# Optimization experiments

Hardware: AMD Instinct MI355X
Metric: run time of the kernel (lower is better)

Reference implementation:

```python
import jax, jax.numpy as jnp
import numpy as np

# ---- static dims (from init_kwargs / Hydra defaults) ----
B_, N_MESH, G, HEADS, DH = 2, 100000, 64, 8, 64
DIM = 256
D_MODEL = HEADS * DH              # 512
EXPAND, D_STATE, D_CONV = 2, 64, 3
D_INNER = EXPAND * D_MODEL        # 1024
HEADDIM = 64
NHEADS = D_INNER // HEADDIM       # 16
CONV_DIM = D_INNER + 2 * D_STATE  # 1152
D_IN_PROJ = 2 * D_INNER + 2 * D_STATE + 2 * NHEADS  # 2208


def _ssd_scan(x, dt, A, B, C):
    """Selective state-space scan (SSD / Mamba2 recurrence).
    x:(bb,L,H,P) dt:(bb,L,H) A:(H,) B,C:(bb,L,N). Returns y:(bb,L,H,P)."""
    bb, L, H, P = x.shape
    N = B.shape[-1]
    xs = jnp.moveaxis(x, 1, 0)   # (L,bb,H,P)
    dts = jnp.moveaxis(dt, 1, 0)  # (L,bb,H)
    Bs = jnp.moveaxis(B, 1, 0)   # (L,bb,N)
    Cs = jnp.moveaxis(C, 1, 0)
    h0 = jnp.zeros((bb, H, P, N), x.dtype)

    def step(h, inp):
        x_t, dt_t, B_t, C_t = inp
        dA = jnp.exp(dt_t * A)                                   # (bb,H)
        h = dA[..., None, None] * h + (dt_t[..., None] * x_t)[..., None] * B_t[:, None, None, :]
        y_t = jnp.einsum('bhpn,bn->bhp', h, C_t)
        return h, y_t

    _, ys = jax.lax.scan(step, h0, (xs, dts, Bs, Cs))
    return jnp.moveaxis(ys, 0, 1)


def _hydra(u, in_proj_w, conv_w, conv_b, dt_bias, A_log, fc_D_w, D, norm_w, out_proj_w):
    """Hydra (bidirectional Mamba2) forward, slow (non mem-eff) path."""
    b, L, _ = u.shape
    zxbcdt = u @ in_proj_w.T                                     # (b,L,2208)
    z = zxbcdt[..., :D_INNER]
    xBC = zxbcdt[..., D_INNER:D_INNER + CONV_DIM]
    dt_raw = zxbcdt[..., D_INNER + CONV_DIM:]                    # (b,L,2*NHEADS)
    # forward heads + time-flipped backward heads stacked along batch
    dt = jnp.concatenate([dt_raw[..., :NHEADS], jnp.flip(dt_raw[..., NHEADS:], axis=1)], axis=0)
    dt = jax.nn.softplus(dt + dt_bias)                           # (2b,L,NHEADS)
    # depthwise non-causal 'same' conv1d + SiLU
    xBC = jax.lax.conv_general_dilated(
        xBC.transpose(0, 2, 1), conv_w, (1,), [(1, 1)],
        dimension_numbers=('NCH', 'OIH', 'NCH'), feature_group_count=CONV_DIM)
    xBC = jax.nn.silu(xBC + conv_b[None, :, None]).transpose(0, 2, 1)
    x = xBC[..., :D_INNER]
    Bc = xBC[..., D_INNER:D_INNER + D_STATE]
    Cc = xBC[..., D_INNER + D_STATE:]
    x_og = x
    x2 = jnp.concatenate([x, jnp.flip(x, 1)], 0).reshape(2 * b, L, NHEADS, HEADDIM)
    B2 = jnp.concatenate([Bc, jnp.flip(Bc, 1)], 0)
    C2 = jnp.concatenate([Cc, jnp.flip(Cc, 1)], 0)
    A = -jnp.exp(A_log)                                          # (NHEADS,)
    y = _ssd_scan(x2, dt, A, B2, C2).reshape(2 * b, L, D_INNER)
    # shift by one (strictly off-diagonal parts), zero first position
    y = jnp.pad(y[:, :-1], ((0, 0), (1, 0), (0, 0)))
    diag = x_og @ fc_D_w.T + D                                   # (b,L,NHEADS)
    y = y[:b] + jnp.flip(y[b:], 1) + x_og * jnp.repeat(diag, HEADDIM, axis=-1)
    # gated RMSNorm
    y = y * jax.nn.silu(z)
    y = y * jax.lax.rsqrt(jnp.mean(y * y, axis=-1, keepdims=True) + 1e-5) * norm_w
    return y @ out_proj_w.T                                      # (b,L,D_MODEL)


def _forward(slice_token, slice_weights, in_proj_w, conv_w, conv_b, dt_bias, A_log,
             fc_D_w, D, norm_w, out_proj_w, to_out_w, to_out_b):
    b, h, g, c = slice_token.shape
    u = slice_token.transpose(0, 2, 1, 3).reshape(b, g, h * c)   # b g (h c)
    out = _hydra(u, in_proj_w, conv_w, conv_b, dt_bias, A_log, fc_D_w, D, norm_w, out_proj_w)
    ost = out.reshape(b, g, h, c).transpose(0, 2, 1, 3)          # b h g c
    out_x = jnp.einsum('bhgc,bhng->bhnc', ost, slice_weights)    # gather back to mesh points
    out_x = out_x.transpose(0, 2, 1, 3).reshape(b, out_x.shape[2], h * c)  # b n (h c)
    return out_x @ to_out_w.T + to_out_b


def setup_inputs() -> dict:
    key = jax.random.key(0)
    ks = jax.random.split(key, 14)
    f32 = jnp.float32
    inp = {}
    inp['slice_token'] = jax.random.normal(ks[0], (B_, HEADS, G, DH), f32)
    inp['slice_weights'] = jax.random.uniform(ks[1], (B_, HEADS, N_MESH, G), f32)
    inp['in_proj_w'] = jax.random.normal(ks[2], (D_IN_PROJ, D_MODEL), f32) * (D_MODEL ** -0.5)
    inp['conv_w'] = jax.random.normal(ks[3], (CONV_DIM, 1, D_CONV), f32) * 0.3
    inp['conv_b'] = jax.random.normal(ks[4], (CONV_DIM,), f32) * 0.02
    inp['dt_bias'] = jnp.log(jnp.expm1(jax.random.uniform(ks[5], (NHEADS,), f32, 0.001, 0.1)))
    inp['A_log'] = jnp.log(jax.random.uniform(ks[6], (NHEADS,), f32, 1.0, 8.0))
    inp['fc_D_w'] = jax.random.normal(ks[7], (NHEADS, D_INNER), f32) * (D_INNER ** -0.5)
    inp['D'] = jax.random.normal(ks[8], (NHEADS,), f32) * 0.1 + 1.0
    inp['norm_w'] = jnp.ones((D_INNER,), f32)
    inp['out_proj_w'] = jax.random.normal(ks[9], (D_MODEL, D_INNER), f32) * (D_INNER ** -0.5)
    inp['to_out_w'] = jax.random.normal(ks[10], (DIM, D_MODEL), f32) * (D_MODEL ** -0.5)
    inp['to_out_b'] = jnp.zeros((DIM,), f32)
    return inp


def reference(slice_token, slice_weights, in_proj_w, conv_w, conv_b, dt_bias, A_log,
              fc_D_w, D, norm_w, out_proj_w, to_out_w, to_out_b):
    return _forward(slice_token, slice_weights, in_proj_w, conv_w, conv_b, dt_bias,
                    A_log, fc_D_w, D, norm_w, out_proj_w, to_out_w, to_out_b)
```

## Files before the change

kernel.cpp:

```cpp
#include <hip/hip_runtime.h>
#include <hip/hip_bf16.h>
#include <math.h>

#define NB 2
#define LL 64
#define NMESH 100000
#define HEADS_O 8
#define DHC 64
#define DMODEL 512
#define DINNER 1024
#define DSTATE 64
#define NH 16
#define CONVDIM 1152
#define DINPROJ 2208
#define DOUT 256
#define NCHUNK 6250

typedef __attribute__((ext_vector_type(8))) short short8v;
typedef __attribute__((ext_vector_type(4))) float f32x4;

__device__ __forceinline__ unsigned short f2bf(float f) {
  union { float f; unsigned u; } v; v.f = f;
  unsigned u = v.u;
  u += 0x7FFFu + ((u >> 16) & 1u);
  return (unsigned short)(u >> 16);
}

__device__ __forceinline__ short8v pack_bf16(float4 lo, float4 hi) {
  short8v r;
  r[0] = (short)f2bf(lo.x); r[1] = (short)f2bf(lo.y);
  r[2] = (short)f2bf(lo.z); r[3] = (short)f2bf(lo.w);
  r[4] = (short)f2bf(hi.x); r[5] = (short)f2bf(hi.y);
  r[6] = (short)f2bf(hi.z); r[7] = (short)f2bf(hi.w);
  return r;
}

__device__ __forceinline__ float dot4(float4 a, const float* b) {
  return a.x*b[0] + a.y*b[1] + a.z*b[2] + a.w*b[3];
}

__device__ __forceinline__ float silu(float s) { return s / (1.f + expf(-s)); }

__global__ void k_inproj(const float* __restrict__ st, const float* __restrict__ w,
                         float* __restrict__ zx) {
  int oc = blockIdx.x;
  int blc = blockIdx.y;
  int t = threadIdx.x;
  __shared__ float u[8][DMODEL];
  for (int idx = t; idx < 8*DMODEL; idx += 256) {
    int r = idx >> 9, m = idx & 511;
    int bl = blc*8 + r; int b = bl >> 6, l = bl & 63;
    u[r][m] = st[((size_t)(b*HEADS_O + (m >> 6))*LL + l)*DHC + (m & 63)];
  }
  __syncthreads();
  int o = oc*256 + t;
  if (o < DINPROJ) {
    const float4* wr = (const float4*)(w + (size_t)o*DMODEL);
    float acc[8] = {0,0,0,0,0,0,0,0};
    for (int m4 = 0; m4 < DMODEL/4; ++m4) {
      float4 wv = wr[m4];
      #pragma unroll
      for (int r = 0; r < 8; ++r) acc[r] += dot4(wv, &u[r][m4*4]);
    }
    #pragma unroll
    for (int r = 0; r < 8; ++r)
      zx[(size_t)(blc*8 + r)*DINPROJ + o] = acc[r];
  }
}

__global__ void k_convdt(const float* __restrict__ zx, const float* __restrict__ cw,
                         const float* __restrict__ cb, const float* __restrict__ dtb,
                         float* __restrict__ conv_out, float* __restrict__ dtbuf) {
  if (blockIdx.x < 576) {
    int i = blockIdx.x*256 + threadIdx.x;
    int c = i % CONVDIM; int l = (i / CONVDIM) % LL; int b = i / (CONVDIM*LL);
    float s = cb[c];
    #pragma unroll
    for (int k = 0; k < 3; ++k) {
      int tt = l - 1 + k;
      if (tt >= 0 && tt < LL)
        s += cw[c*3 + k] * zx[(size_t)(b*LL + tt)*DINPROJ + DINNER + c];
    }
    conv_out[i] = silu(s);
  } else {
    int i = (blockIdx.x - 576)*256 + threadIdx.x;
    if (i < 4*LL*NH) {
      int h = i & 15, l = (i >> 4) & 63, s = i >> 10;
      float v;
      if (s < 2)
        v = zx[(size_t)(s*LL + l)*DINPROJ + (DINNER + CONVDIM) + h];
      else
        v = zx[(size_t)((s-2)*LL + (63-l))*DINPROJ + (DINNER + CONVDIM) + 16 + h];
      v += dtb[h];
      dtbuf[i] = (v > 20.f) ? v : log1pf(expf(v));
    }
  }
}

__global__ void k_scan(const float* __restrict__ conv_out, const float* __restrict__ dtbuf,
                       const float* __restrict__ A_log, float* __restrict__ ybuf) {
  int blk = blockIdx.x;
  int s = blk >> 4, hh = blk & 15;
  int b = s & 1;
  bool rev = (s >= 2);
  int t = threadIdx.x;
  int wv = t >> 6, lane = t & 63;
  __shared__ float Bs[64*68];
  __shared__ float Cs[64*68];
  __shared__ float Xs[64*64];
  __shared__ float dts[64];
  __shared__ float Dc[64];

  for (int id = t; id < 4096; id += 256) {
    int tt0 = id >> 6, n = id & 63;
    int tt = rev ? (63 - tt0) : tt0;
    size_t base = (size_t)(b*LL + tt) * CONVDIM;
    Xs[tt0*64 + n] = conv_out[base + hh*64 + n];
    Bs[tt0*68 + n] = conv_out[base + DINNER + n];
    Cs[tt0*68 + n] = conv_out[base + DINNER + DSTATE + n];
  }
  if (t < 64) dts[t] = dtbuf[(size_t)(s*LL + t)*NH + hh];
  __syncthreads();
  if (t < 64) {
    float v = dts[t];
    #pragma unroll
    for (int m = 1; m < 64; m <<= 1) {
      float o = __shfl_up(v, m, 64);
      if (lane >= m) v += o;
    }
    Dc[t] = v;
  }
  __syncthreads();
  float A = -expf(A_log[hh]);
  float g[16];
  #pragma unroll
  for (int i = 0; i < 16; ++i) {
    int tt = wv + 4*i;
    int ta = lane;
    float gv = 0.f;
    if (ta <= tt) {
      const float* Br = &Bs[ta*68];
      const float* Cr = &Cs[tt*68];
      float dot = 0.f;
      #pragma unroll
      for (int n4 = 0; n4 < 16; ++n4) {
        float4 bv = *(const float4*)&Br[n4*4];
        float4 cv = *(const float4*)&Cr[n4*4];
        dot += bv.x*cv.x + bv.y*cv.y + bv.z*cv.z + bv.w*cv.w;
      }
      gv = dot * expf(A * (Dc[tt] - Dc[ta])) * dts[ta];
    }
    g[i] = gv;
  }
  __syncthreads();
  #pragma unroll
  for (int i = 0; i < 16; ++i) Bs[(wv + 4*i)*64 + lane] = g[i];
  __syncthreads();
  for (int id = t; id < 4096; id += 256) {
    int tt = id >> 6, p = id & 63;
    float y = 0.f;
    for (int ta = 0; ta <= tt; ++ta) y += Bs[tt*64 + ta] * Xs[ta*64 + p];
    ybuf[(size_t)(s*LL + tt)*DINNER + hh*64 + p] = y;
  }
}

__global__ void k_norm(const float* __restrict__ conv_out, const float* __restrict__ zx,
                       const float* __restrict__ yb, const float* __restrict__ fcD,
                       const float* __restrict__ Dd, const float* __restrict__ nw,
                       float* __restrict__ ynorm) {
  int bl = blockIdx.x; int b = bl >> 6, l = bl & 63;
  int t = threadIdx.x;
  __shared__ float xog[DINNER];
  __shared__ float diag[NH];
  __shared__ float wsum[4];
  size_t base = (size_t)bl * CONVDIM;
  for (int c = t; c < DINNER; c += 256) xog[c] = conv_out[base + c];
  __syncthreads();
  {
    int hh = t >> 4, j = t & 15;
    const float* fr = fcD + (size_t)hh*DINNER;
    float acc = 0.f;
    for (int k = 0; k < 64; ++k) acc += xog[j + 16*k] * fr[j + 16*k];
    #pragma unroll
    for (int m = 8; m >= 1; m >>= 1) acc += __shfl_xor(acc, m, 64);
    if (j == 0) diag[hh] = acc + Dd[hh];
  }
  __syncthreads();
  float ss = 0.f;
  float y2v[4];
  #pragma unroll
  for (int i = 0; i < 4; ++i) {
    int c = t + 256*i;
    float yf = (l == 0)  ? 0.f : yb[(size_t)(b*LL + l - 1)*DINNER + c];
    float yw = (l == 63) ? 0.f : yb[(size_t)((2+b)*LL + 62 - l)*DINNER + c];
    float y1 = yf + yw + xog[c]*diag[c >> 6];
    float z = zx[(size_t)bl*DINPROJ + c];
    float y2 = y1 * silu(z);
    y2v[i] = y2;
    ss += y2*y2;
  }
  #pragma unroll
  for (int m = 32; m >= 1; m >>= 1) ss += __shfl_xor(ss, m, 64);
  if ((t & 63) == 0) wsum[t >> 6] = ss;
  __syncthreads();
  float tot = wsum[0] + wsum[1] + wsum[2] + wsum[3];
  float scale = rsqrtf(tot * (1.f/1024.f) + 1e-5f);
  #pragma unroll
  for (int i = 0; i < 4; ++i) {
    int c = t + 256*i;
    ynorm[(size_t)bl*DINNER + c] = y2v[i] * scale * nw[c];
  }
}

__global__ void k_oproj(const float* __restrict__ ynorm, const float* __restrict__ opw,
                        float* __restrict__ oh) {
  int oc = blockIdx.x;
  int blc = blockIdx.y;
  int t = threadIdx.x;
  __shared__ float yr[4][DINNER];
  for (int idx = t; idx < 4*DINNER; idx += 256) {
    int r = idx >> 10, k = idx & 1023;
    yr[r][k] = ynorm[(size_t)(blc*4 + r)*DINNER + k];
  }
  __syncthreads();
  int o = oc*256 + t;
  const float4* wr = (const float4*)(opw + (size_t)o*DINNER);
  float acc[4] = {0,0,0,0};
  for (int k4 = 0; k4 < DINNER/4; ++k4) {
    float4 wv = wr[k4];
    #pragma unroll
    for (int r = 0; r < 4; ++r) acc[r] += dot4(wv, &yr[r][k4*4]);
  }
  #pragma unroll
  for (int r = 0; r < 4; ++r)
    oh[(size_t)(blc*4 + r)*DMODEL + o] = acc[r];
}

__global__ void k_mfrag(const float* __restrict__ oh, const float* __restrict__ tow,
                        unsigned short* __restrict__ mfp) {
  int bgc = blockIdx.x;
  int dc  = blockIdx.y;
  int t = threadIdx.x;
  __shared__ float orow[8][DMODEL];
  for (int idx = t; idx < 8*DMODEL; idx += 256) {
    int r = idx >> 9, m = idx & 511;
    orow[r][m] = oh[(size_t)(bgc*8 + r)*DMODEL + m];
  }
  __syncthreads();
  #pragma unroll
  for (int ii = 0; ii < 2; ++ii) {
    int idx = t + 256*ii;
    int h = idx >> 6, dl = idx & 63;
    int d = dc*64 + dl;
    const float4* wr = (const float4*)(tow + (size_t)d*DMODEL + h*64);
    float acc[8] = {0,0,0,0,0,0,0,0};
    #pragma unroll
    for (int c4 = 0; c4 < 16; ++c4) {
      float4 wv = wr[c4];
      #pragma unroll
      for (int r = 0; r < 8; ++r) acc[r] += dot4(wv, &orow[r][h*64 + c4*4]);
    }
    #pragma unroll
    for (int r = 0; r < 8; ++r) {
      int bg = bgc*8 + r; int b = bg >> 6, g = bg & 63;
      int kk = g >> 5;
      int ln = (d & 15) | (((g & 31) >> 3) << 4);
      int j = g & 7;
      mfp[((((size_t)(b*HEADS_O + h)*2 + kk)*16 + (d >> 4))*64 + ln)*8 + j] = f2bf(acc[r]);
    }
  }
}

__global__ __launch_bounds__(512, 1) void k_out_gemm(const float* __restrict__ W,
                                                     const unsigned short* __restrict__ mf,
                                                     const float* __restrict__ tob,
                                                     float* __restrict__ out) {
  int bx = blockIdx.x;
  int b    = bx >> 7;
  int base = bx & 127;
  int tid = threadIdx.x;
  int wv = tid >> 6, lane = tid & 63;
  int r16 = lane & 15, kg = lane >> 4;

  __shared__ __align__(16) unsigned short lsA[2][16][512];

  short8v B0[16], B1[16];
  {
    const unsigned short* mfb = mf + (size_t)b*(16*16*512) + lane*8;
    #pragma unroll
    for (int ks = 0; ks < 16; ++ks) {
      B0[ks] = *(const short8v*)(mfb + ((size_t)ks*16 + 2*wv    )*512);
      B1[ks] = *(const short8v*)(mfb + ((size_t)ks*16 + 2*wv + 1)*512);
    }
  }
  float bias0 = tob[wv*32 + r16];
  float bias1 = tob[wv*32 + 16 + r16];

  const float* wbase = W + ((size_t)(b*HEADS_O + wv)*NMESH + r16)*64 + kg*8;

  float4 s00, s01, s10, s11;
  #define ALOAD(cc) do { \
    const float* p0 = wbase + (size_t)(cc)*1024; \
    s00 = *(const float4*)p0;        s01 = *(const float4*)(p0 + 4); \
    s10 = *(const float4*)(p0 + 32); s11 = *(const float4*)(p0 + 36); \
  } while (0)
  #define AWRITE(pp) do { \
    *(short8v*)&lsA[pp][2*wv    ][lane*8] = pack_bf16(s00, s01); \
    *(short8v*)&lsA[pp][2*wv + 1][lane*8] = pack_bf16(s10, s11); \
  } while (0)

  ALOAD(base);
  AWRITE(0);
  asm volatile("s_waitcnt lgkmcnt(0)" ::: "memory");
  __builtin_amdgcn_sched_barrier(0);
  __builtin_amdgcn_s_barrier();
  __builtin_amdgcn_sched_barrier(0);

  int c = base;
  int p = 0;
  for (;;) {
    int cn = c + 128;
    bool more = (cn < NCHUNK);
    if (more) ALOAD(cn);
    __builtin_amdgcn_sched_barrier(0);

    f32x4 acc0 = (f32x4){0.f,0.f,0.f,0.f};
    f32x4 acc1 = (f32x4){0.f,0.f,0.f,0.f};
    #pragma unroll
    for (int ks = 0; ks < 16; ++ks) {
      short8v af = *(const short8v*)&lsA[p][ks][lane*8];
      acc0 = __builtin_amdgcn_mfma_f32_16x16x32_bf16(af, B0[ks], acc0, 0, 0, 0);
      acc1 = __builtin_amdgcn_mfma_f32_16x16x32_bf16(af, B1[ks], acc1, 0, 0, 0);
    }

    int rb = c*16 + kg*4;
    int cg = wv*32 + r16;
    #pragma unroll
    for (int r = 0; r < 4; ++r) {
      out[((size_t)b*NMESH + rb + r)*DOUT + cg]      = acc0[r] + bias0;
      out[((size_t)b*NMESH + rb + r)*DOUT + cg + 16] = acc1[r] + bias1;
    }

    if (!more) break;
    __builtin_amdgcn_sched_barrier(0);
    AWRITE(p ^ 1);
    asm volatile("s_waitcnt lgkmcnt(0)" ::: "memory");
    __builtin_amdgcn_sched_barrier(0);
    __builtin_amdgcn_s_barrier();
    __builtin_amdgcn_sched_barrier(0);
    p ^= 1;
    c = cn;
  }
  #undef ALOAD
  #undef AWRITE
}

extern "C" void kernel_launch(void* const* d_in, const int* in_sizes, int n_in,
                              void* d_out, int out_size, void* d_ws, size_t ws_size,
                              hipStream_t stream) {
  (void)in_sizes; (void)n_in; (void)out_size; (void)ws_size;
  const float* st   = (const float*)d_in[0];
  const float* sw   = (const float*)d_in[1];
  const float* ipw  = (const float*)d_in[2];
  const float* cw   = (const float*)d_in[3];
  const float* cb   = (const float*)d_in[4];
  const float* dtb  = (const float*)d_in[5];
  const float* alog = (const float*)d_in[6];
  const float* fcD  = (const float*)d_in[7];
  const float* Dd   = (const float*)d_in[8];
  const float* nw   = (const float*)d_in[9];
  const float* opw  = (const float*)d_in[10];
  const float* tow  = (const float*)d_in[11];
  const float* tob  = (const float*)d_in[12];
  float* out = (float*)d_out;
  unsigned char* ws = (unsigned char*)d_ws;

  float* zx   = (float*)(ws + 0);
  float* conv = (float*)(ws + 1130496);
  float* dtp  = (float*)(ws + 1720320);
  float* yb   = (float*)(ws + 1736704);
  float* ynm  = (float*)(ws + 2785280);
  float* oh   = (float*)(ws + 3309568);
  unsigned short* mfr = (unsigned short*)(ws + 3571712);

  k_inproj  <<<dim3(9, 16), 256, 0, stream>>>(st, ipw, zx);
  k_convdt  <<<592, 256, 0, stream>>>(zx, cw, cb, dtb, conv, dtp);
  k_scan    <<<64,  256, 0, stream>>>(conv, dtp, alog, yb);
  k_norm    <<<128, 256, 0, stream>>>(conv, zx, yb, fcD, Dd, nw, ynm);
  k_oproj   <<<dim3(2, 32), 256, 0, stream>>>(ynm, opw, oh);
  k_mfrag   <<<dim3(16, 4), 256, 0, stream>>>(oh, tow, mfr);
  k_out_gemm<<<256, 512, 0, stream>>>(sw, mfr, tob, out);
}
```

Before: 241.9 us.

## Process two 16-row chunks per iteration in output GEMM to halve barriers

The final output GEMM now handles 32 mesh rows per loop iteration instead of 16. It loads twice as much slice-weight data per prefetch and issues four MFMA accumulator chains. The grid changes from 256 to 250 blocks so that 125 blocks per batch evenly cover 3125 chunks. This halves the number of barriers and loop iterations and exposes more memory-level parallelism per wave, at the cost of more registers and twice the LDS buffer size.

```diff
diff --git a/kernel.cpp b/kernel.cpp
--- a/kernel.cpp
+++ b/kernel.cpp
@@ -14,7 +14,7 @@
 #define CONVDIM 1152
 #define DINPROJ 2208
 #define DOUT 256
-#define NCHUNK 6250
+#define NC32 3125
 
 typedef __attribute__((ext_vector_type(8))) short short8v;
 typedef __attribute__((ext_vector_type(4))) float f32x4;
@@ -276,13 +276,13 @@
                                                      const float* __restrict__ tob,
                                                      float* __restrict__ out) {
   int bx = blockIdx.x;
-  int b    = bx >> 7;
-  int base = bx & 127;
+  int b    = bx / 125;
+  int base = bx % 125;
   int tid = threadIdx.x;
   int wv = tid >> 6, lane = tid & 63;
   int r16 = lane & 15, kg = lane >> 4;
 
-  __shared__ __align__(16) unsigned short lsA[2][16][512];
+  __shared__ __align__(16) unsigned short lsA[2][2][16][512];
 
   short8v B0[16], B1[16];
   {
@@ -298,61 +298,78 @@
 
   const float* wbase = W + ((size_t)(b*HEADS_O + wv)*NMESH + r16)*64 + kg*8;
 
-  float4 s00, s01, s10, s11;
-  #define ALOAD(cc) do { \
-    const float* p0 = wbase + (size_t)(cc)*1024; \
-    s00 = *(const float4*)p0;        s01 = *(const float4*)(p0 + 4); \
-    s10 = *(const float4*)(p0 + 32); s11 = *(const float4*)(p0 + 36); \
+  float4 t0, t1, t2, t3, t4, t5, t6, t7;
+
+  #define ALOADS(CC) do { \
+    const float* p0 = wbase + (size_t)(CC)*2048; \
+    t0 = *(const float4*)p0;          t1 = *(const float4*)(p0 + 4); \
+    t2 = *(const float4*)(p0 + 32);   t3 = *(const float4*)(p0 + 36); \
+    t4 = *(const float4*)(p0 + 1024); t5 = *(const float4*)(p0 + 1028); \
+    t6 = *(const float4*)(p0 + 1056); t7 = *(const float4*)(p0 + 1060); \
   } while (0)
-  #define AWRITE(pp) do { \
-    *(short8v*)&lsA[pp][2*wv    ][lane*8] = pack_bf16(s00, s01); \
-    *(short8v*)&lsA[pp][2*wv + 1][lane*8] = pack_bf16(s10, s11); \
+  #define AWR(pp) do { \
+    *(short8v*)&lsA[pp][0][2*wv    ][lane*8] = pack_bf16(t0, t1); \
+    *(short8v*)&lsA[pp][0][2*wv + 1][lane*8] = pack_bf16(t2, t3); \
+    *(short8v*)&lsA[pp][1][2*wv    ][lane*8] = pack_bf16(t4, t5); \
+    *(short8v*)&lsA[pp][1][2*wv + 1][lane*8] = pack_bf16(t6, t7); \
   } while (0)
-
-  ALOAD(base);
-  AWRITE(0);
-  asm volatile("s_waitcnt lgkmcnt(0)" ::: "memory");
-  __builtin_amdgcn_sched_barrier(0);
-  __builtin_amdgcn_s_barrier();
-  __builtin_amdgcn_sched_barrier(0);
-
-  int c = base;
+  #define KBAR() do { \
+    asm volatile("s_waitcnt lgkmcnt(0)" ::: "memory"); \
+    __builtin_amdgcn_sched_barrier(0); \
+    __builtin_amdgcn_s_barrier(); \
+    __builtin_amdgcn_sched_barrier(0); \
+  } while (0)
+
+  ALOADS(base);
+  AWR(0);
+  KBAR();
+
+  int C = base;
   int p = 0;
   for (;;) {
-    int cn = c + 128;
-    bool more = (cn < NCHUNK);
-    if (more) ALOAD(cn);
+    int Cn = C + 125;
+    bool more = (Cn < NC32);
+    if (more) ALOADS(Cn);
     __builtin_amdgcn_sched_barrier(0);
 
-    f32x4 acc0 = (f32x4){0.f,0.f,0.f,0.f};
-    f32x4 acc1 = (f32x4){0.f,0.f,0.f,0.f};
+    f32x4 a00 = (f32x4){0.f,0.f,0.f,0.f};
+    f32x4 a01 = (f32x4){0.f,0.f,0.f,0.f};
+    f32x4 a10 = (f32x4){0.f,0.f,0.f,0.f};
+    f32x4 a11 = (f32x4){0.f,0.f,0.f,0.f};
     #pragma unroll
     for (int ks = 0; ks < 16; ++ks) {
-      short8v af = *(const short8v*)&lsA[p][ks][lane*8];
-      acc0 = __builtin_amdgcn_mfma_f32_16x16x32_bf16(af, B0[ks], acc0, 0, 0, 0);
-      acc1 = __builtin_amdgcn_mfma_f32_16x16x32_bf16(af, B1[ks], acc1, 0, 0, 0);
-    }
-
-    int rb = c*16 + kg*4;
-    int cg = wv*32 + r16;
-    #pragma unroll
-    for (int r = 0; r < 4; ++r) {
-      out[((size_t)b*NMESH + rb + r)*DOUT + cg]      = acc0[r] + bias0;
-      out[((size_t)b*NMESH + rb + r)*DOUT + cg + 16] = acc1[r] + bias1;
+      short8v af0 = *(const short8v*)&lsA[p][0][ks][lane*8];
+      short8v af1 = *(const short8v*)&lsA[p][1][ks][lane*8];
+      a00 = __builtin_amdgcn_mfma_f32_16x16x32_bf16(af0, B0[ks], a00, 0, 0, 0);
+      a01 = __builtin_amdgcn_mfma_f32_16x16x32_bf16(af0, B1[ks], a01, 0, 0, 0);
+      a10 = __builtin_amdgcn_mfma_f32_16x16x32_bf16(af1, B0[ks], a10, 0, 0, 0);
+      a11 = __builtin_amdgcn_mfma_f32_16x16x32_bf16(af1, B1[ks], a11, 0, 0, 0);
+    }
+
+    {
+      int rb0 = C*32 + kg*4;
+      int cg = wv*32 + r16;
+      #pragma unroll
+      for (int r = 0; r < 4; ++r) {
+        size_t ro0 = ((size_t)b*NMESH + rb0 + r)*DOUT;
+        size_t ro1 = ((size_t)b*NMESH + rb0 + 16 + r)*DOUT;
+        out[ro0 + cg]      = a00[r] + bias0;
+        out[ro0 + cg + 16] = a01[r] + bias1;
+        out[ro1 + cg]      = a10[r] + bias0;
+        out[ro1 + cg + 16] = a11[r] + bias1;
+      }
     }
 
     if (!more) break;
     __builtin_amdgcn_sched_barrier(0);
-    AWRITE(p ^ 1);
-    asm volatile("s_waitcnt lgkmcnt(0)" ::: "memory");
-    __builtin_amdgcn_sched_barrier(0);
-    __builtin_amdgcn_s_barrier();
-    __builtin_amdgcn_sched_barrier(0);
+    AWR(p ^ 1);
+    KBAR();
     p ^= 1;
-    c = cn;
-  }
-  #undef ALOAD
-  #undef AWRITE
+    C = Cn;
+  }
+  #undef ALOADS
+  #undef AWR
+  #undef KBAR
 }
 
 extern "C" void kernel_launch(void* const* d_in, const int* in_sizes, int n_in,
@@ -389,5 +406,5 @@
   k_norm    <<<128, 256, 0, stream>>>(conv, zx, yb, fcD, Dd, nw, ynm);
   k_oproj   <<<dim3(2, 32), 256, 0, stream>>>(ynm, opw, oh);
   k_mfrag   <<<dim3(16, 4), 256, 0, stream>>>(oh, tow, mfr);
-  k_out_gemm<<<256, 512, 0, stream>>>(sw, mfr, tob, out);
-}
+  k_out_gemm<<<250, 512, 0, stream>>>(sw, mfr, tob, out);
+}
```

After: 245.1 us. No clear change (+1.3%).
